# Performance work log

Measured on AMD Instinct MI355X. Metric: run time of the kernel, lower is better.

Reference implementation:

```python
import jax, jax.numpy as jnp
import numpy as np

DEPTH = 6
N_LEAF = 2 ** DEPTH          # 64
GATE_COUNT = N_LEAF - 1      # 63
IN_F = 512
OUT_F = 512
BATCH = 1024


def setup_inputs() -> dict:
    key = jax.random.key(0)
    k1, k2, k3 = jax.random.split(key, 3)
    x = jax.random.normal(k1, (BATCH, IN_F), dtype=jnp.float32)
    gw = jax.random.normal(k2, (IN_F, GATE_COUNT), dtype=jnp.float32)
    gb = jnp.zeros((GATE_COUNT,), dtype=jnp.float32)
    pw = jax.random.normal(k3, (OUT_F, IN_F, N_LEAF), dtype=jnp.float32)
    pb = jnp.zeros((OUT_F, N_LEAF), dtype=jnp.float32)
    return {"x": x, "gw": gw, "gb": gb, "pw": pw, "pb": pb}


def _leaf_probs(x, gw, gb, depth):
    # gatings: sigmoid(x @ gw + gb), shape [B, gate_count]
    g = jax.nn.sigmoid(x @ gw + gb)
    B = x.shape[0]
    dens = jnp.ones((B, 1), dtype=x.dtype)  # root density
    offset = 0
    for d in range(depth):
        n = 2 ** d
        gp = g[:, offset:offset + n]                    # parent gatings [B, n]
        # left child multiplies by g, right child by (1 - g), interleaved
        pair = jnp.stack([gp, 1.0 - gp], axis=-1).reshape(B, 2 * n)
        dens = jnp.repeat(dens, 2, axis=1) * pair        # [B, 2n]
        offset += n
    return dens  # [B, n_leaf]


def reference(x, gw, gb, pw, pb):
    leaf = _leaf_probs(x, gw, gb, DEPTH)                 # [B, L]
    # per-leaf linear projections, then mix with leaf probabilities
    y = jnp.einsum('bi,oil->bol', x, pw)                 # [B, O, L]
    out = jnp.einsum('bol,bl->bo', y, leaf) + leaf @ pb.T
    return out
```

## Files before the change

kernel.cpp:

```cpp
#include <hip/hip_runtime.h>
#include <hip/hip_bf16.h>

#define TDEPTH 6
#define NLEAF 64
#define NGATE 63
#define INF 512
#define OUTF 512
#define BATCH 1024

#define BM 128
#define BN 64
#define SPLITK 16
#define THREADS 128
#define NPL 32

typedef __attribute__((ext_vector_type(4)))  float f32x4;
typedef __attribute__((ext_vector_type(16))) float f32x16;
typedef __attribute__((ext_vector_type(8)))  __bf16 bf16x8;

__device__ __forceinline__ bf16x8 pack8(f32x4 a, f32x4 b) {
  bf16x8 w;
  w[0] = (__bf16)a[0]; w[1] = (__bf16)a[1];
  w[2] = (__bf16)a[2]; w[3] = (__bf16)a[3];
  w[4] = (__bf16)b[0]; w[5] = (__bf16)b[1];
  w[6] = (__bf16)b[2]; w[7] = (__bf16)b[3];
  return w;
}

__global__ __launch_bounds__(256) void prep_kernel(
    const float* __restrict__ x, const float* __restrict__ gw,
    const float* __restrict__ gb, const float* __restrict__ pw,
    float* __restrict__ leaf, __bf16* __restrict__ pwb) {
  const int tid = threadIdx.x;
  if (blockIdx.x < 256) {
    const int wid = tid >> 6, lane = tid & 63;
    const int b = blockIdx.x * 4 + wid;
    __shared__ float g[4][NLEAF];
    if (lane < NGATE) {
      const float* xr = x + (size_t)b * INF;
      float a0 = 0.f, a1 = 0.f, a2 = 0.f, a3 = 0.f;
      #pragma unroll 4
      for (int i = 0; i < INF; i += 4) {
        a0 += xr[i + 0] * gw[(i + 0) * NGATE + lane];
        a1 += xr[i + 1] * gw[(i + 1) * NGATE + lane];
        a2 += xr[i + 2] * gw[(i + 2) * NGATE + lane];
        a3 += xr[i + 3] * gw[(i + 3) * NGATE + lane];
      }
      float t = (a0 + a1) + (a2 + a3) + gb[lane];
      g[wid][lane] = 1.0f / (1.0f + __expf(-t));
    }
    __syncthreads();
    float p = 1.0f;
    #pragma unroll
    for (int d = 0; d < TDEPTH; d++) {
      int prefix = lane >> (TDEPTH - 1 - d);
      int node = (1 << d) - 1 + (prefix >> 1);
      float gv = g[wid][node];
      p *= (prefix & 1) ? (1.0f - gv) : gv;
    }
    leaf[(size_t)b * NLEAF + lane] = p;
  } else {
    const unsigned Q = (blockIdx.x - 256) * 256 + tid;
    const unsigned tile = Q >> 9;
    const unsigned nb = tile >> 9, i = tile & 511;
    const unsigned q = Q & 511;
    const unsigned r = ((q >> 7) << 3) + ((q >> 4) & 7);
    const unsigned v = (q & 15) ^ (r & 15);
    const unsigned o = nb * 64 + ((v >> 3) << 5) + r;
    const unsigned kg = v & 7;
    const float* src = pw + ((size_t)o * INF + i) * NLEAF + kg * 8;
    f32x4 a = *(const f32x4*)src, b = *(const f32x4*)(src + 4);
    *(bf16x8*)((char*)pwb + (size_t)Q * 16) = pack8(a, b);
  }
}

__device__ __forceinline__ void gload_lds16(const void* g, void* l) {
  __builtin_amdgcn_global_load_lds(
      (const __attribute__((address_space(1))) void*)g,
      (__attribute__((address_space(3))) void*)l, 16, 0, 0);
}

__global__ __launch_bounds__(THREADS, 2) void gemm_kernel(
    const __bf16* __restrict__ pwb, const float* __restrict__ pb,
    const float* __restrict__ x, const float* __restrict__ leaf,
    float* __restrict__ partial) {
  __shared__ __align__(16) __bf16 Bsm[3][32 * 128];
  __shared__ __align__(16) __bf16 xsm[NPL][BM];

  const int tid = threadIdx.x, lane = tid & 63, w = tid >> 6;
  const int lo = lane & 31, half = lane >> 5;

  const int L = (blockIdx.x & 7) * 128 + (blockIdx.x >> 3);
  const int mb = L & 7;
  const int rest = L >> 3;
  const int nb = rest & 7, s = rest >> 3;
  const int m0 = mb * BM, n0 = nb * BN;
  const int cs = s * NPL;

  f32x4 lf[2][4][2];
  #pragma unroll
  for (int mt = 0; mt < 2; mt++) {
    const float* lr =
        leaf + (size_t)(m0 + w * 64 + mt * 32 + lo) * NLEAF + half * 8;
    #pragma unroll
    for (int t4 = 0; t4 < 4; t4++) {
      lf[mt][t4][0] = *(const f32x4*)(lr + t4 * 16);
      lf[mt][t4][1] = *(const f32x4*)(lr + t4 * 16 + 4);
    }
  }

  {
    const float* src = x + (size_t)(m0 + tid) * INF + cs;
    #pragma unroll
    for (int c4 = 0; c4 < NPL / 4; c4++) {
      f32x4 v = *(const f32x4*)(src + c4 * 4);
      #pragma unroll
      for (int j = 0; j < 4; j++) xsm[c4 * 4 + j][tid] = (__bf16)v[j];
    }
  }

  const char* pwc = (const char*)pwb;
  const size_t tbase = (size_t)(nb * 512 + cs) << 13;

  auto stage = [&](char* dstb, int t) {
    const char* srcb = pwc + tbase + ((size_t)t << 13);
    #pragma unroll
    for (int j = 0; j < 4; j++)
      gload_lds16(srcb + j * 2048 + tid * 16, dstb + j * 2048 + w * 1024);
  };

  f32x16 acc00 = (f32x16)(0.f), acc01 = (f32x16)(0.f);
  f32x16 acc10 = (f32x16)(0.f), acc11 = (f32x16)(0.f);
  const unsigned swz = (unsigned)(lo & 15) << 4;

  auto do_step = [&](const char* bufc, int t) {
    const float xv0 = (float)xsm[t][w * 64 + lo];
    const float xv1 = (float)xsm[t][w * 64 + 32 + lo];
    #pragma unroll
    for (int t4 = 0; t4 < 4; t4++) {
      const unsigned kb0 = ((unsigned)(t4 * 32 + half * 16)) ^ swz;
      const unsigned kb1 = ((unsigned)(128 + t4 * 32 + half * 16)) ^ swz;
      bf16x8 bf0 = *(const bf16x8*)(bufc + lo * 256 + kb0);
      bf16x8 bf1 = *(const bf16x8*)(bufc + lo * 256 + kb1);
      f32x4 p0a = lf[0][t4][0] * xv0, p0b = lf[0][t4][1] * xv0;
      f32x4 p1a = lf[1][t4][0] * xv1, p1b = lf[1][t4][1] * xv1;
      bf16x8 a0 = pack8(p0a, p0b);
      bf16x8 a1 = pack8(p1a, p1b);
      acc00 = __builtin_amdgcn_mfma_f32_32x32x16_bf16(a0, bf0, acc00, 0, 0, 0);
      acc01 = __builtin_amdgcn_mfma_f32_32x32x16_bf16(a0, bf1, acc01, 0, 0, 0);
      acc10 = __builtin_amdgcn_mfma_f32_32x32x16_bf16(a1, bf0, acc10, 0, 0, 0);
      acc11 = __builtin_amdgcn_mfma_f32_32x32x16_bf16(a1, bf1, acc11, 0, 0, 0);
    }
  };

  char* bA = (char*)&Bsm[0][0];
  char* bB = (char*)&Bsm[1][0];
  char* bC = (char*)&Bsm[2][0];

  stage(bA, 0);
  stage(bB, 1);
  __builtin_amdgcn_sched_barrier(0);
  asm volatile("s_waitcnt vmcnt(4) lgkmcnt(0)" ::: "memory");
  __builtin_amdgcn_s_barrier();
  __builtin_amdgcn_sched_barrier(0);

  for (int t = 0; t < NPL - 2; ++t) {
    stage(bC, t + 2);
    do_step(bA, t);
    __builtin_amdgcn_sched_barrier(0);
    asm volatile("s_waitcnt vmcnt(4) lgkmcnt(0)" ::: "memory");
    __builtin_amdgcn_s_barrier();
    __builtin_amdgcn_sched_barrier(0);
    char* tmp = bA; bA = bB; bB = bC; bC = tmp;
  }
  do_step(bA, NPL - 2);
  __builtin_amdgcn_sched_barrier(0);
  asm volatile("s_waitcnt vmcnt(0) lgkmcnt(0)" ::: "memory");
  __builtin_amdgcn_s_barrier();
  __builtin_amdgcn_sched_barrier(0);
  do_step(bB, NPL - 1);

  if (s == SPLITK - 1) {
    #pragma unroll
    for (int t4 = 0; t4 < 4; t4++) {
      bf16x8 a0 = pack8(lf[0][t4][0], lf[0][t4][1]);
      bf16x8 a1 = pack8(lf[1][t4][0], lf[1][t4][1]);
      #pragma unroll
      for (int nt = 0; nt < 2; nt++) {
        const float* pr =
            pb + (size_t)(n0 + nt * 32 + lo) * NLEAF + t4 * 16 + half * 8;
        f32x4 c0 = *(const f32x4*)pr, c1 = *(const f32x4*)(pr + 4);
        bf16x8 bb = pack8(c0, c1);
        if (nt == 0) {
          acc00 = __builtin_amdgcn_mfma_f32_32x32x16_bf16(a0, bb, acc00, 0, 0, 0);
          acc10 = __builtin_amdgcn_mfma_f32_32x32x16_bf16(a1, bb, acc10, 0, 0, 0);
        } else {
          acc01 = __builtin_amdgcn_mfma_f32_32x32x16_bf16(a0, bb, acc01, 0, 0, 0);
          acc11 = __builtin_amdgcn_mfma_f32_32x32x16_bf16(a1, bb, acc11, 0, 0, 0);
        }
      }
    }
  }

  #pragma unroll
  for (int mt = 0; mt < 2; mt++) {
    float* dst =
        partial + ((size_t)s * BATCH + m0 + w * 64 + mt * 32) * OUTF + n0;
    #pragma unroll
    for (int e = 0; e < 16; e++) {
      int row = (e & 3) + 8 * (e >> 2) + 4 * half;
      if (mt == 0) {
        dst[(size_t)row * OUTF + lo] = acc00[e];
        dst[(size_t)row * OUTF + 32 + lo] = acc01[e];
      } else {
        dst[(size_t)row * OUTF + lo] = acc10[e];
        dst[(size_t)row * OUTF + 32 + lo] = acc11[e];
      }
    }
  }
}

__global__ __launch_bounds__(256) void reduce_kernel(
    const float* __restrict__ partial, float* __restrict__ out) {
  size_t e = ((size_t)blockIdx.x * 256 + threadIdx.x) * 4;
  f32x4 sum = (f32x4){0.f, 0.f, 0.f, 0.f};
  #pragma unroll
  for (int s = 0; s < SPLITK; s++)
    sum += *(const f32x4*)(partial + (size_t)s * BATCH * OUTF + e);
  *(f32x4*)(out + e) = sum;
}

extern "C" void kernel_launch(void* const* d_in, const int* in_sizes, int n_in,
                              void* d_out, int out_size, void* d_ws, size_t ws_size,
                              hipStream_t stream) {
  const float* x  = (const float*)d_in[0];
  const float* gw = (const float*)d_in[1];
  const float* gb = (const float*)d_in[2];
  const float* pw = (const float*)d_in[3];
  const float* pb = (const float*)d_in[4];
  float* out = (float*)d_out;

  float*  leaf    = (float*)d_ws;
  __bf16* pwb     = (__bf16*)((char*)d_ws + (1 << 20));
  float*  partial = (float*)((char*)d_ws + (33ull << 20));

  prep_kernel<<<256 + 8192, 256, 0, stream>>>(x, gw, gb, pw, leaf, pwb);
  gemm_kernel<<<8 * 8 * SPLITK, THREADS, 0, stream>>>(pwb, pb, x, leaf, partial);
  reduce_kernel<<<(BATCH * OUTF) / (256 * 4), 256, 0, stream>>>(partial, out);
}
```

Measured before the change: 75.39 us.

## Factor x out of the leaf contraction and fold pb bias into the weight tiles

The GEMM inner step is restructured. Each step computes pw_tile·leaf with the leaf fragment held as a constant bf16 MFMA operand, then scales the fp32 result by the per-row x value. This replaces forming x*leaf products and packing them to bf16 on every step. The bias pb is appended to the repacked weight as an extra 513th input row with x=1, which removes the special bias epilogue. The output tile narrows to 32 columns with occupancy 4, partials are stored transposed, and the reduce kernel transposes through LDS. The trade-offs are more blocks, extra MFMAs per unit of output (each x column now needs its own small reduction), and a more complex reduction.

Result: no change. 75.68 us (+0.4%).

```diff
diff --git a/kernel.cpp b/kernel.cpp
--- a/kernel.cpp
+++ b/kernel.cpp
@@ -9,7 +9,7 @@
 #define BATCH 1024
 
 #define BM 128
-#define BN 64
+#define BN 32
 #define SPLITK 16
 #define THREADS 128
 #define NPL 32
@@ -30,7 +30,8 @@
 __global__ __launch_bounds__(256) void prep_kernel(
     const float* __restrict__ x, const float* __restrict__ gw,
     const float* __restrict__ gb, const float* __restrict__ pw,
-    float* __restrict__ leaf, __bf16* __restrict__ pwb) {
+    const float* __restrict__ pb, float* __restrict__ leaf,
+    __bf16* __restrict__ pwb) {
   const int tid = threadIdx.x;
   if (blockIdx.x < 256) {
     const int wid = tid >> 6, lane = tid & 63;
@@ -61,14 +62,15 @@
     leaf[(size_t)b * NLEAF + lane] = p;
   } else {
     const unsigned Q = (blockIdx.x - 256) * 256 + tid;
-    const unsigned tile = Q >> 9;
-    const unsigned nb = tile >> 9, i = tile & 511;
-    const unsigned q = Q & 511;
-    const unsigned r = ((q >> 7) << 3) + ((q >> 4) & 7);
-    const unsigned v = (q & 15) ^ (r & 15);
-    const unsigned o = nb * 64 + ((v >> 3) << 5) + r;
-    const unsigned kg = v & 7;
-    const float* src = pw + ((size_t)o * INF + i) * NLEAF + kg * 8;
+    const unsigned tile = Q >> 8;
+    const unsigned nb32 = tile / 513;
+    const unsigned i = tile - nb32 * 513;
+    const unsigned q = Q & 255;
+    const unsigned r = q >> 3;
+    const unsigned g = (q & 7) ^ (r & 7);
+    const unsigned o = nb32 * 32 + r;
+    const float* src = (i < INF) ? (pw + ((size_t)o * INF + i) * NLEAF + g * 8)
+                                 : (pb + (size_t)o * NLEAF + g * 8);
     f32x4 a = *(const f32x4*)src, b = *(const f32x4*)(src + 4);
     *(bf16x8*)((char*)pwb + (size_t)Q * 16) = pack8(a, b);
   }
@@ -80,33 +82,32 @@
       (__attribute__((address_space(3))) void*)l, 16, 0, 0);
 }
 
-__global__ __launch_bounds__(THREADS, 2) void gemm_kernel(
-    const __bf16* __restrict__ pwb, const float* __restrict__ pb,
-    const float* __restrict__ x, const float* __restrict__ leaf,
-    float* __restrict__ partial) {
-  __shared__ __align__(16) __bf16 Bsm[3][32 * 128];
+__global__ __launch_bounds__(THREADS, 4) void gemm_kernel(
+    const __bf16* __restrict__ pwb, const float* __restrict__ x,
+    const float* __restrict__ leaf, float* __restrict__ partial) {
+  __shared__ __align__(16) __bf16 Bsm[3][2048];
   __shared__ __align__(16) __bf16 xsm[NPL][BM];
 
   const int tid = threadIdx.x, lane = tid & 63, w = tid >> 6;
   const int lo = lane & 31, half = lane >> 5;
 
-  const int L = (blockIdx.x & 7) * 128 + (blockIdx.x >> 3);
+  const int L = ((int)blockIdx.x & 7) * 256 + ((int)blockIdx.x >> 3);
   const int mb = L & 7;
   const int rest = L >> 3;
-  const int nb = rest & 7, s = rest >> 3;
-  const int m0 = mb * BM, n0 = nb * BN;
+  const int nb = rest & 15, s = rest >> 4;
+  const int m0 = mb * BM, o0 = nb * BN;
   const int cs = s * NPL;
-
-  f32x4 lf[2][4][2];
+  const int count = NPL + (s == SPLITK - 1 ? 1 : 0);
+
+  bf16x8 lfb[2][4];
   #pragma unroll
   for (int mt = 0; mt < 2; mt++) {
     const float* lr =
         leaf + (size_t)(m0 + w * 64 + mt * 32 + lo) * NLEAF + half * 8;
     #pragma unroll
-    for (int t4 = 0; t4 < 4; t4++) {
-      lf[mt][t4][0] = *(const f32x4*)(lr + t4 * 16);
-      lf[mt][t4][1] = *(const f32x4*)(lr + t4 * 16 + 4);
-    }
+    for (int t4 = 0; t4 < 4; t4++)
+      lfb[mt][t4] = pack8(*(const f32x4*)(lr + t4 * 16),
+                          *(const f32x4*)(lr + t4 * 16 + 4));
   }
 
   {
@@ -119,37 +120,42 @@
     }
   }
 
-  const char* pwc = (const char*)pwb;
-  const size_t tbase = (size_t)(nb * 512 + cs) << 13;
+  const char* tb = (const char*)pwb + ((size_t)(nb * 513 + cs) << 12);
 
   auto stage = [&](char* dstb, int t) {
-    const char* srcb = pwc + tbase + ((size_t)t << 13);
-    #pragma unroll
-    for (int j = 0; j < 4; j++)
-      gload_lds16(srcb + j * 2048 + tid * 16, dstb + j * 2048 + w * 1024);
+    const char* srcb = tb + ((size_t)t << 12);
+    #pragma unroll
+    for (int rnd = 0; rnd < 2; rnd++)
+      gload_lds16(srcb + rnd * 2048 + tid * 16, dstb + rnd * 2048 + w * 1024);
   };
 
-  f32x16 acc00 = (f32x16)(0.f), acc01 = (f32x16)(0.f);
-  f32x16 acc10 = (f32x16)(0.f), acc11 = (f32x16)(0.f);
-  const unsigned swz = (unsigned)(lo & 15) << 4;
+  f32x16 acc0 = (f32x16)(0.f), acc1 = (f32x16)(0.f);
+  const unsigned swz = (unsigned)(lo & 7) << 4;
 
   auto do_step = [&](const char* bufc, int t) {
-    const float xv0 = (float)xsm[t][w * 64 + lo];
-    const float xv1 = (float)xsm[t][w * 64 + 32 + lo];
-    #pragma unroll
-    for (int t4 = 0; t4 < 4; t4++) {
-      const unsigned kb0 = ((unsigned)(t4 * 32 + half * 16)) ^ swz;
-      const unsigned kb1 = ((unsigned)(128 + t4 * 32 + half * 16)) ^ swz;
-      bf16x8 bf0 = *(const bf16x8*)(bufc + lo * 256 + kb0);
-      bf16x8 bf1 = *(const bf16x8*)(bufc + lo * 256 + kb1);
-      f32x4 p0a = lf[0][t4][0] * xv0, p0b = lf[0][t4][1] * xv0;
-      f32x4 p1a = lf[1][t4][0] * xv1, p1b = lf[1][t4][1] * xv1;
-      bf16x8 a0 = pack8(p0a, p0b);
-      bf16x8 a1 = pack8(p1a, p1b);
-      acc00 = __builtin_amdgcn_mfma_f32_32x32x16_bf16(a0, bf0, acc00, 0, 0, 0);
-      acc01 = __builtin_amdgcn_mfma_f32_32x32x16_bf16(a0, bf1, acc01, 0, 0, 0);
-      acc10 = __builtin_amdgcn_mfma_f32_32x32x16_bf16(a1, bf0, acc10, 0, 0, 0);
-      acc11 = __builtin_amdgcn_mfma_f32_32x32x16_bf16(a1, bf1, acc11, 0, 0, 0);
+    float xv0 = 1.0f, xv1 = 1.0f;
+    if (t < NPL) {
+      xv0 = (float)xsm[t][w * 64 + lo];
+      xv1 = (float)xsm[t][w * 64 + 32 + lo];
+    }
+    bf16x8 af[4];
+    #pragma unroll
+    for (int t4 = 0; t4 < 4; t4++)
+      af[t4] = *(const bf16x8*)(bufc + lo * 128 +
+                                (((unsigned)(t4 * 32 + half * 16)) ^ swz));
+    {
+      f32x16 D = (f32x16)(0.f);
+      #pragma unroll
+      for (int t4 = 0; t4 < 4; t4++)
+        D = __builtin_amdgcn_mfma_f32_32x32x16_bf16(af[t4], lfb[0][t4], D, 0, 0, 0);
+      acc0 += D * xv0;
+    }
+    {
+      f32x16 D = (f32x16)(0.f);
+      #pragma unroll
+      for (int t4 = 0; t4 < 4; t4++)
+        D = __builtin_amdgcn_mfma_f32_32x32x16_bf16(af[t4], lfb[1][t4], D, 0, 0, 0);
+      acc1 += D * xv1;
     }
   };
 
@@ -160,74 +166,62 @@
   stage(bA, 0);
   stage(bB, 1);
   __builtin_amdgcn_sched_barrier(0);
-  asm volatile("s_waitcnt vmcnt(4) lgkmcnt(0)" ::: "memory");
+  asm volatile("s_waitcnt vmcnt(2) lgkmcnt(0)" ::: "memory");
   __builtin_amdgcn_s_barrier();
   __builtin_amdgcn_sched_barrier(0);
 
-  for (int t = 0; t < NPL - 2; ++t) {
+  for (int t = 0; t < count - 2; ++t) {
     stage(bC, t + 2);
     do_step(bA, t);
     __builtin_amdgcn_sched_barrier(0);
-    asm volatile("s_waitcnt vmcnt(4) lgkmcnt(0)" ::: "memory");
+    asm volatile("s_waitcnt vmcnt(2) lgkmcnt(0)" ::: "memory");
     __builtin_amdgcn_s_barrier();
     __builtin_amdgcn_sched_barrier(0);
     char* tmp = bA; bA = bB; bB = bC; bC = tmp;
   }
-  do_step(bA, NPL - 2);
+  do_step(bA, count - 2);
   __builtin_amdgcn_sched_barrier(0);
   asm volatile("s_waitcnt vmcnt(0) lgkmcnt(0)" ::: "memory");
   __builtin_amdgcn_s_barrier();
   __builtin_amdgcn_sched_barrier(0);
-  do_step(bB, NPL - 1);
-
-  if (s == SPLITK - 1) {
-    #pragma unroll
-    for (int t4 = 0; t4 < 4; t4++) {
-      bf16x8 a0 = pack8(lf[0][t4][0], lf[0][t4][1]);
-      bf16x8 a1 = pack8(lf[1][t4][0], lf[1][t4][1]);
-      #pragma unroll
-      for (int nt = 0; nt < 2; nt++) {
-        const float* pr =
-            pb + (size_t)(n0 + nt * 32 + lo) * NLEAF + t4 * 16 + half * 8;
-        f32x4 c0 = *(const f32x4*)pr, c1 = *(const f32x4*)(pr + 4);
-        bf16x8 bb = pack8(c0, c1);
-        if (nt == 0) {
-          acc00 = __builtin_amdgcn_mfma_f32_32x32x16_bf16(a0, bb, acc00, 0, 0, 0);
-          acc10 = __builtin_amdgcn_mfma_f32_32x32x16_bf16(a1, bb, acc10, 0, 0, 0);
-        } else {
-          acc01 = __builtin_amdgcn_mfma_f32_32x32x16_bf16(a0, bb, acc01, 0, 0, 0);
-          acc11 = __builtin_amdgcn_mfma_f32_32x32x16_bf16(a1, bb, acc11, 0, 0, 0);
-        }
-      }
-    }
-  }
+  do_step(bB, count - 1);
 
   #pragma unroll
   for (int mt = 0; mt < 2; mt++) {
-    float* dst =
-        partial + ((size_t)s * BATCH + m0 + w * 64 + mt * 32) * OUTF + n0;
+    float* dstb = partial + ((size_t)s * OUTF + o0) * BATCH +
+                  (m0 + w * 64 + mt * 32);
+    const f32x16 a = mt ? acc1 : acc0;
     #pragma unroll
     for (int e = 0; e < 16; e++) {
       int row = (e & 3) + 8 * (e >> 2) + 4 * half;
-      if (mt == 0) {
-        dst[(size_t)row * OUTF + lo] = acc00[e];
-        dst[(size_t)row * OUTF + 32 + lo] = acc01[e];
-      } else {
-        dst[(size_t)row * OUTF + lo] = acc10[e];
-        dst[(size_t)row * OUTF + 32 + lo] = acc11[e];
-      }
+      dstb[(size_t)row * BATCH + lo] = a[e];
     }
   }
 }
 
 __global__ __launch_bounds__(256) void reduce_kernel(
     const float* __restrict__ partial, float* __restrict__ out) {
-  size_t e = ((size_t)blockIdx.x * 256 + threadIdx.x) * 4;
-  f32x4 sum = (f32x4){0.f, 0.f, 0.f, 0.f};
-  #pragma unroll
-  for (int s = 0; s < SPLITK; s++)
-    sum += *(const f32x4*)(partial + (size_t)s * BATCH * OUTF + e);
-  *(f32x4*)(out + e) = sum;
+  __shared__ float tile[32][65];
+  const int t = threadIdx.x;
+  const int O0 = ((int)blockIdx.x >> 4) * 32;
+  const int B0 = ((int)blockIdx.x & 15) * 64;
+  #pragma unroll
+  for (int rep = 0; rep < 8; rep++) {
+    const int idx = rep * 256 + t;
+    const int o = idx >> 6, b = idx & 63;
+    float sum = 0.f;
+    #pragma unroll
+    for (int s = 0; s < SPLITK; s++)
+      sum += partial[((size_t)s * OUTF + O0 + o) * BATCH + B0 + b];
+    tile[o][b] = sum;
+  }
+  __syncthreads();
+  #pragma unroll
+  for (int rep = 0; rep < 8; rep++) {
+    const int idx = rep * 256 + t;
+    const int b = idx >> 5, o = idx & 31;
+    out[(size_t)(B0 + b) * OUTF + O0 + o] = tile[o][b];
+  }
 }
 
 extern "C" void kernel_launch(void* const* d_in, const int* in_sizes, int n_in,
@@ -241,10 +235,10 @@
   float* out = (float*)d_out;
 
   float*  leaf    = (float*)d_ws;
-  __bf16* pwb     = (__bf16*)((char*)d_ws + (1 << 20));
-  float*  partial = (float*)((char*)d_ws + (33ull << 20));
-
-  prep_kernel<<<256 + 8192, 256, 0, stream>>>(x, gw, gb, pw, leaf, pwb);
-  gemm_kernel<<<8 * 8 * SPLITK, THREADS, 0, stream>>>(pwb, pb, x, leaf, partial);
-  reduce_kernel<<<(BATCH * OUTF) / (256 * 4), 256, 0, stream>>>(partial, out);
-}
+  __bf16* pwb     = (__bf16*)((char*)d_ws + (256 << 10));
+  float*  partial = (float*)((char*)d_ws + (256 << 10) + (size_t)16 * 513 * 4096);
+
+  prep_kernel<<<256 + 8208, 256, 0, stream>>>(x, gw, gb, pw, pb, leaf, pwb);
+  gemm_kernel<<<8 * 16 * SPLITK, THREADS, 0, stream>>>(pwb, x, leaf, partial);
+  reduce_kernel<<<256, 256, 0, stream>>>(partial, out);
+}
```
